# Kernel tuning notes

Hardware: AMD Instinct MI355X
Metric: run time of the kernel (lower is better)

## Reference

```python
import jax, jax.numpy as jnp
import numpy as np

D_MODEL = 512
NUM_HEADS = 8
D_HEAD = D_MODEL // NUM_HEADS
SCALE = 1.0 / np.sqrt(D_HEAD)


def setup_inputs() -> dict:
    key = jax.random.key(0)
    ks = jax.random.split(key, 16)
    B, T, D = 8, 1024, D_MODEL
    std = 1.0 / np.sqrt(D)
    inp = {
        'x': jax.random.normal(ks[0], (B, T, D), jnp.float32),
        'pos_enc': jax.random.normal(ks[1], (1, 2 * T - 1, D), jnp.float32),
        'Wq': jax.random.normal(ks[2], (D, D), jnp.float32) * std,
        'bq': jnp.zeros((D,), jnp.float32),
        'Wk': jax.random.normal(ks[3], (D, D), jnp.float32) * std,
        'bk': jnp.zeros((D,), jnp.float32),
        'Wv': jax.random.normal(ks[4], (D, D), jnp.float32) * std,
        'bv': jnp.zeros((D,), jnp.float32),
        'Wpos': jax.random.normal(ks[5], (D, D), jnp.float32) * std,
        'pos_bias_u': jax.random.normal(ks[6], (NUM_HEADS, D_HEAD), jnp.float32) * std,
        'pos_bias_v': jax.random.normal(ks[7], (NUM_HEADS, D_HEAD), jnp.float32) * std,
        'Wo': jax.random.normal(ks[8], (D, D), jnp.float32) * std,
        'bo': jnp.zeros((D,), jnp.float32),
    }
    return inp


def _relative_shift(x):
    # x: (batch, heads, time, 2*time-1) -> (batch, heads, time, time)
    b, h, t, _ = x.shape
    x = jnp.pad(x, ((0, 0), (0, 0), (0, 0), (1, 0)))  # (b,h,t,2t)
    x = x.reshape(b, h, 2 * t, t)
    x = x[:, :, 1:, :]
    x = x.reshape(b, h, t, 2 * t - 1)
    return x[:, :, :, :t]


def reference(x, pos_enc, Wq, bq, Wk, bk, Wv, bv, Wpos, pos_bias_u, pos_bias_v, Wo, bo):
    B, T, D = x.shape
    H, Dh = NUM_HEADS, D_HEAD
    q = (x @ Wq + bq).reshape(B, T, H, Dh).transpose(0, 2, 1, 3)  # (B,H,T,Dh)
    k = (x @ Wk + bk).reshape(B, T, H, Dh).transpose(0, 2, 1, 3)
    v = (x @ Wv + bv).reshape(B, T, H, Dh).transpose(0, 2, 1, 3)
    p = (pos_enc @ Wpos).reshape(1, -1, H, Dh).transpose(0, 2, 1, 3)  # (1,H,2T-1,Dh)

    q_u = q + pos_bias_u[None, :, None, :]
    q_v = q + pos_bias_v[None, :, None, :]

    content_score = jnp.einsum('bhtd,bhsd->bhts', q_u, k)         # (B,H,T,T)
    pos_score = jnp.einsum('bhtd,xhpd->bhtp', q_v, p)             # (B,H,T,2T-1)
    pos_score = _relative_shift(pos_score)                         # (B,H,T,T)

    scores = (content_score + pos_score) * SCALE
    attn = jax.nn.softmax(scores, axis=-1)
    out = jnp.einsum('bhts,bhsd->bhtd', attn, v)                   # (B,H,T,Dh)
    out = out.transpose(0, 2, 1, 3).reshape(B, T, D)
    return out @ Wo + bo
```

## Files before the change

kernel.cpp:

```cpp
#include <hip/hip_runtime.h>
#include <hip/hip_bf16.h>

#define T_SEQ 1024
#define D_MODEL 512
#define N_HEADS 8
#define D_HEAD 64
#define KSCALE 0.1803368801111244f

typedef unsigned short ushort_t;
typedef short s16x8 __attribute__((ext_vector_type(8)));
typedef float f32x4 __attribute__((ext_vector_type(4)));

__device__ inline f32x4 mfma16(s16x8 a, s16x8 b, f32x4 c) {
    return __builtin_amdgcn_mfma_f32_16x16x32_bf16(a, b, c, 0, 0, 0);
}

__device__ inline ushort_t f2bf(float f) {
    union { float f; unsigned u; } v; v.f = f;
    unsigned r = v.u + 0x7FFFu + ((v.u >> 16) & 1u);
    return (ushort_t)(r >> 16);
}
__device__ inline float bf2f(short s) {
    union { unsigned u; float f; } t; t.u = ((unsigned)(unsigned short)s) << 16; return t.f;
}
__device__ inline void cvt4(const float4 f, ushort_t* t) {
    t[0] = f2bf(f.x); t[1] = f2bf(f.y); t[2] = f2bf(f.z); t[3] = f2bf(f.w);
}
__device__ inline s16x8 pack8(const ushort_t* t) {
    s16x8 r;
    #pragma unroll
    for (int e = 0; e < 8; ++e) r[e] = (short)t[e];
    return r;
}

__device__ inline int lidx(int row, int chunk) {
    return row * 64 + ((chunk ^ (row & 7)) << 3);
}

__device__ inline void gl_lds16(const ushort_t* g, ushort_t* l) {
    __builtin_amdgcn_global_load_lds(
        (const __attribute__((address_space(1))) unsigned*)g,
        (__attribute__((address_space(3))) unsigned*)l, 16, 0, 0);
}

__global__ __launch_bounds__(256) void prep(
    const float* __restrict__ x, const float* __restrict__ pos,
    const float* __restrict__ W0, const float* __restrict__ W1,
    const float* __restrict__ W2, const float* __restrict__ W3,
    const float* __restrict__ W4,
    ushort_t* __restrict__ xb, ushort_t* __restrict__ posb,
    ushort_t* __restrict__ WT)
{
    __shared__ float T[64][68];
    const int bx = blockIdx.x;
    const int tid = threadIdx.x;
    if (bx < 2560) {
        const size_t N1 = (size_t)8192 * 512;
        size_t e = ((size_t)bx * 256 + tid) * 8;
        ushort_t tmp[8];
        if (e < N1) {
            const float4* s = (const float4*)(x + e);
            cvt4(s[0], tmp); cvt4(s[1], tmp + 4);
            *(s16x8*)(xb + e) = pack8(tmp);
        } else {
            size_t e2 = e - N1;
            int row = (int)(e2 >> 9);
            if (row < 2047) {
                const float4* s = (const float4*)(pos + e2);
                cvt4(s[0], tmp); cvt4(s[1], tmp + 4);
            } else {
                #pragma unroll
                for (int i = 0; i < 8; ++i) tmp[i] = 0;
            }
            *(s16x8*)(posb + e2) = pack8(tmp);
        }
    } else {
        const int bz = bx - 2560;
        const int z = bz >> 6;
        const int rem = bz & 63;
        const int n0 = (rem & 7) * 64, k0 = (rem >> 3) * 64;
        const float* W = (z == 0) ? W0 : (z == 1) ? W1
                       : (z == 2) ? W2 : (z == 3) ? W3 : W4;
        const int rr = tid >> 2, cc = (tid & 3) * 16;

        const float* src = W + (size_t)(k0 + rr) * 512 + n0 + cc;
        *(float4*)&T[rr][cc + 0]  = *(const float4*)(src);
        *(float4*)&T[rr][cc + 4]  = *(const float4*)(src + 4);
        *(float4*)&T[rr][cc + 8]  = *(const float4*)(src + 8);
        *(float4*)&T[rr][cc + 12] = *(const float4*)(src + 12);
        __syncthreads();

        ushort_t tmp[16];
        #pragma unroll
        for (int e = 0; e < 16; ++e) tmp[e] = f2bf(T[cc + e][rr]);
        ushort_t* dst = WT + ((size_t)z * 512 + n0 + rr) * 512 + k0 + cc;
        *(s16x8*)dst       = pack8(tmp);
        *(s16x8*)(dst + 8) = pack8(tmp + 8);
    }
}

__global__ __launch_bounds__(256) void gemm_qkvp(
    const ushort_t* __restrict__ xb, const ushort_t* __restrict__ posb,
    const ushort_t* __restrict__ WT,
    const float* __restrict__ bq, const float* __restrict__ bk,
    const float* __restrict__ bv, const float* __restrict__ pbu,
    ushort_t* __restrict__ Qu, ushort_t* __restrict__ Ko,
    ushort_t* __restrict__ VoT, ushort_t* __restrict__ Po)
{
    const int tid = threadIdx.x;
    const int flat = blockIdx.x;
    const int nf = (flat & 7) * 104 + (flat >> 3);
    const int bxi = nf % 13, byi = nf / 13;

    const bool is_p = (bxi == 12);
    int row0, col0;
    const ushort_t* A;
    const ushort_t* B;
    if (is_p) {
        row0 = (byi >> 2) * 128;
        col0 = (byi & 3) * 128;
        A = posb;
        B = WT + (size_t)3 * 512 * 512;
    } else {
        row0 = byi * 128;
        col0 = bxi * 128;
        A = xb;
        B = WT;
    }
    const int w = tid >> 6, lane = tid & 63;
    const int quad = lane >> 4, lanelo = lane & 15;
    const int wr = w >> 1, wc = w & 1;

    __shared__ ushort_t AsF[2][128 * 64];
    __shared__ ushort_t BsF[2][128 * 64];

    const int rs = tid >> 3, js = (tid & 7) * 8;
    const size_t lofs = (size_t)(tid & ~63) * 8;

    f32x4 acc[4][4] = {};

    #pragma unroll
    for (int i = 0; i < 4; ++i) {
        gl_lds16(A + (size_t)(row0 + i * 32 + rs) * 512 + js,
                 AsF[0] + (size_t)i * 2048 + lofs);
        gl_lds16(B + (size_t)(col0 + i * 32 + rs) * 512 + js,
                 BsF[0] + (size_t)i * 2048 + lofs);
    }

    for (int kk = 0; kk < 8; ++kk) {
        const int cur = kk & 1;
        __syncthreads();
        if (kk < 7) {
            const int k1 = (kk + 1) * 64;
            #pragma unroll
            for (int i = 0; i < 4; ++i) {
                gl_lds16(A + (size_t)(row0 + i * 32 + rs) * 512 + k1 + js,
                         AsF[cur ^ 1] + (size_t)i * 2048 + lofs);
                gl_lds16(B + (size_t)(col0 + i * 32 + rs) * 512 + k1 + js,
                         BsF[cur ^ 1] + (size_t)i * 2048 + lofs);
            }
        }
        const ushort_t* Ac = AsF[cur];
        const ushort_t* Bc = BsF[cur];
        #pragma unroll
        for (int ks = 0; ks < 2; ++ks) {
            s16x8 af[4], bf[4];
            #pragma unroll
            for (int i = 0; i < 4; ++i)
                af[i] = *(const s16x8*)(Ac + (size_t)(64 * wr + 16 * i + lanelo) * 64 + ks * 32 + quad * 8);
            #pragma unroll
            for (int j = 0; j < 4; ++j)
                bf[j] = *(const s16x8*)(Bc + (size_t)(64 * wc + 16 * j + lanelo) * 64 + ks * 32 + quad * 8);
            #pragma unroll
            for (int i = 0; i < 4; ++i)
                #pragma unroll
                for (int j = 0; j < 4; ++j)
                    acc[i][j] = mfma16(af[i], bf[j], acc[i][j]);
        }
    }

    if (is_p) {
        #pragma unroll
        for (int j = 0; j < 4; ++j) {
            int c = col0 + 64 * wc + 16 * j + lanelo;
            #pragma unroll
            for (int i = 0; i < 4; ++i)
                #pragma unroll
                for (int r = 0; r < 4; ++r) {
                    int row = row0 + 64 * wr + 16 * i + 4 * quad + r;
                    Po[(size_t)row * 512 + c] = f2bf(acc[i][j][r]);
                }
        }
        return;
    }

    const int set = col0 >> 9;
    const int cbase = (col0 & 511) + 64 * wc;
    if (set == 0) {
        #pragma unroll
        for (int j = 0; j < 4; ++j) {
            int c = cbase + 16 * j + lanelo;
            float vq = bq[c] + pbu[c];
            #pragma unroll
            for (int i = 0; i < 4; ++i)
                #pragma unroll
                for (int r = 0; r < 4; ++r) {
                    int row = row0 + 64 * wr + 16 * i + 4 * quad + r;
                    Qu[(size_t)row * 512 + c] = f2bf((acc[i][j][r] + vq) * KSCALE);
                }
        }
    } else if (set == 1) {
        #pragma unroll
        for (int j = 0; j < 4; ++j) {
            int c = cbase + 16 * j + lanelo;
            float vbk = bk[c];
            #pragma unroll
            for (int i = 0; i < 4; ++i)
                #pragma unroll
                for (int r = 0; r < 4; ++r) {
                    int row = row0 + 64 * wr + 16 * i + 4 * quad + r;
                    Ko[(size_t)row * 512 + c] = f2bf(acc[i][j][r] + vbk);
                }
        }
    } else {
        const int b_idx = row0 >> 10;
        #pragma unroll
        for (int j = 0; j < 4; ++j) {
            int c = cbase + 16 * j + lanelo;
            int hh = c >> 6, d = c & 63;
            float vbb = bv[c];
            #pragma unroll
            for (int i = 0; i < 4; ++i) {
                int t = (row0 & 1023) + 64 * wr + 16 * i + 4 * quad;
                ushort4 vp;
                vp.x = f2bf(acc[i][j][0] + vbb);
                vp.y = f2bf(acc[i][j][1] + vbb);
                vp.z = f2bf(acc[i][j][2] + vbb);
                vp.w = f2bf(acc[i][j][3] + vbb);
                *(ushort4*)(VoT + ((size_t)((b_idx * 8 + hh) * 64 + d)) * 1024 + t) = vp;
            }
        }
    }
}

__global__ __launch_bounds__(256, 2) void attn_mfma(
    const ushort_t* __restrict__ Qu,
    const ushort_t* __restrict__ Kb, const ushort_t* __restrict__ VT,
    const ushort_t* __restrict__ Pb,
    const float* __restrict__ pbu, const float* __restrict__ pbv,
    ushort_t* __restrict__ AOb)
{
    const int tid = threadIdx.x;
    const int flat = blockIdx.x;
    const int nf = (flat & 7) * 64 + (flat >> 3);
    const int t0 = (nf & 7) * 128;
    const int h  = (nf >> 3) & 7;
    const int b  = nf >> 6;

    const int w = tid >> 6, lane = tid & 63;
    const int quad = lane >> 4, lanelo = lane & 15;

    __shared__ ushort_t Kt[2 * 64 * 64];
    __shared__ ushort_t VtT[2 * 64 * 64];
    __shared__ ushort_t Pt[256 * 64];
    __shared__ ushort_t Ps[128 * 64];

    const size_t qr0 = (size_t)(b * T_SEQ + t0 + 32 * w + lanelo) * 512 + h * 64;
    s16x8 qu0[2], qu1[2], qv0[2], qv1[2];
    qu0[0] = *(const s16x8*)(Qu + qr0 + quad * 8);
    qu0[1] = *(const s16x8*)(Qu + qr0 + 32 + quad * 8);
    qu1[0] = *(const s16x8*)(Qu + qr0 + (size_t)16 * 512 + quad * 8);
    qu1[1] = *(const s16x8*)(Qu + qr0 + (size_t)16 * 512 + 32 + quad * 8);
    #pragma unroll
    for (int e = 0; e < 8; ++e) {
        int k0i = h * 64 + quad * 8 + e;
        float d0 = (pbv[k0i] - pbu[k0i]) * KSCALE;
        float d1 = (pbv[k0i + 32] - pbu[k0i + 32]) * KSCALE;
        qv0[0][e] = (short)f2bf(bf2f(qu0[0][e]) + d0);
        qv0[1][e] = (short)f2bf(bf2f(qu0[1][e]) + d1);
        qv1[0][e] = (short)f2bf(bf2f(qu1[0][e]) + d0);
        qv1[1][e] = (short)f2bf(bf2f(qu1[1][e]) + d1);
    }

    f32x4 acc_o[2][4] = {};
    float l_part[2][4] = {{0.f,0.f,0.f,0.f},{0.f,0.f,0.f,0.f}};

    const ushort_t* VTbh = VT + ((size_t)((b * 8 + h) * 64)) * 1024;
    const ushort_t* Kbh  = Kb + (size_t)b * T_SEQ * 512 + (size_t)h * 64;
    const int pr_base = 960 - t0;

    {
        #pragma unroll
        for (int i = 0; i < 2; ++i) {
            const int L = i * 256 + tid;
            const int r = L >> 3;
            const int ch = (L & 7) ^ (r & 7);
            gl_lds16(Kbh + (size_t)r * 512 + ch * 8,
                     Kt + (size_t)(i * 256 + (tid & ~63)) * 8);
            gl_lds16(VTbh + (size_t)r * 1024 + ch * 8,
                     VtT + (size_t)(i * 256 + (tid & ~63)) * 8);
        }
        const int g0p = pr_base - 64;
        #pragma unroll
        for (int i = 0; i < 6; ++i) {
            const int L = i * 256 + tid;
            const int gr = g0p + (L >> 3);
            const int ch = (L & 7) ^ (gr & 7);
            const int sgb = (g0p + ((i * 256 + (tid & ~63)) >> 3)) & 255;
            gl_lds16(Pb + (size_t)gr * 512 + h * 64 + ch * 8,
                     Pt + (size_t)sgb * 64);
        }
    }
    __syncthreads();

    for (int it = 0; it < 16; ++it) {
        const int s0 = it * 64;
        const int cur = it & 1;

        if (it < 15) {
            ushort_t* Kn = Kt + (cur ^ 1) * 4096;
            ushort_t* Vn = VtT + (cur ^ 1) * 4096;
            const int sn = s0 + 64;
            #pragma unroll
            for (int i = 0; i < 2; ++i) {
                const int L = i * 256 + tid;
                const int r = L >> 3;
                const int ch = (L & 7) ^ (r & 7);
                gl_lds16(Kbh + (size_t)(sn + r) * 512 + ch * 8,
                         Kn + (size_t)(i * 256 + (tid & ~63)) * 8);
                gl_lds16(VTbh + (size_t)r * 1024 + sn + ch * 8,
                         Vn + (size_t)(i * 256 + (tid & ~63)) * 8);
            }
            const int g0 = pr_base + s0 + 128;
            #pragma unroll
            for (int i = 0; i < 2; ++i) {
                const int L = i * 256 + tid;
                const int gr = g0 + (L >> 3);
                const int ch = (L & 7) ^ (gr & 7);
                const int sgb = (g0 + ((i * 256 + (tid & ~63)) >> 3)) & 255;
                gl_lds16(Pb + (size_t)gr * 512 + h * 64 + ch * 8,
                         Pt + (size_t)sgb * 64);
            }
        }

        const ushort_t* Kc = Kt + cur * 4096;
        const ushort_t* Vc = VtT + cur * 4096;
        const int pb = (pr_base + s0) & 255;

        f32x4 acc_c[2][4] = {};
        f32x4 acc_g[2][5] = {};
        __builtin_amdgcn_s_setprio(1);
        #pragma unroll
        for (int ks = 0; ks < 2; ++ks) {
            #pragma unroll
            for (int tn = 0; tn < 4; ++tn) {
                s16x8 kf = *(const s16x8*)(Kc + lidx(tn * 16 + lanelo, 4 * ks + quad));
                acc_c[0][tn] = mfma16(qu0[ks], kf, acc_c[0][tn]);
                acc_c[1][tn] = mfma16(qu1[ks], kf, acc_c[1][tn]);
            }
            #pragma unroll
            for (int m = 0; m < 6; ++m) {
                int prow = (pb + 256 + (2 - 2 * w + m) * 16 + lanelo) & 255;
                s16x8 pf = *(const s16x8*)(Pt + lidx(prow, 4 * ks + quad));
                if (m >= 1) acc_g[0][m - 1] = mfma16(qv0[ks], pf, acc_g[0][m - 1]);
                if (m <= 4) acc_g[1][m]     = mfma16(qv1[ks], pf, acc_g[1][m]);
            }
        }
        __builtin_amdgcn_s_setprio(0);

        #pragma unroll
        for (int rt = 0; rt < 2; ++rt) {
            #pragma unroll
            for (int r = 0; r < 4; ++r) {
                const int u = lanelo + 15 - 4 * quad - r;
                const int srcl = (quad << 4) | (u & 15);
                const bool hi = (u >= 16);
                #pragma unroll
                for (int tn = 0; tn < 4; ++tn) {
                    float v0 = __shfl(acc_g[rt][tn][r], srcl);
                    float v1 = __shfl(acc_g[rt][tn + 1][r], srcl);
                    float e = __builtin_amdgcn_exp2f(acc_c[rt][tn][r] + (hi ? v1 : v0));
                    l_part[rt][r] += e;
                    const int pr = 32 * w + 16 * rt + 4 * quad + r;
                    const int ch = 2 * tn + (lanelo >> 3);
                    Ps[pr * 64 + ((ch ^ (pr & 7)) << 3) + (lanelo & 7)] = f2bf(e);
                }
            }
        }
        asm volatile("s_waitcnt lgkmcnt(0)" ::: "memory");

        __builtin_amdgcn_s_setprio(1);
        #pragma unroll
        for (int ks = 0; ks < 2; ++ks) {
            s16x8 af0 = *(const s16x8*)(Ps + lidx(32 * w + lanelo, 4 * ks + quad));
            s16x8 af1 = *(const s16x8*)(Ps + lidx(32 * w + 16 + lanelo, 4 * ks + quad));
            #pragma unroll
            for (int dt = 0; dt < 4; ++dt) {
                s16x8 vb = *(const s16x8*)(Vc + lidx(dt * 16 + lanelo, 4 * ks + quad));
                acc_o[0][dt] = mfma16(af0, vb, acc_o[0][dt]);
                acc_o[1][dt] = mfma16(af1, vb, acc_o[1][dt]);
            }
        }
        __builtin_amdgcn_s_setprio(0);

        __syncthreads();
    }

    float inv[2][4];
    #pragma unroll
    for (int rt = 0; rt < 2; ++rt)
        #pragma unroll
        for (int r = 0; r < 4; ++r) {
            float l = l_part[rt][r];
            l += __shfl_xor(l, 1);
            l += __shfl_xor(l, 2);
            l += __shfl_xor(l, 4);
            l += __shfl_xor(l, 8);
            inv[rt][r] = 1.0f / l;
        }

    #pragma unroll
    for (int rt = 0; rt < 2; ++rt)
        #pragma unroll
        for (int dt = 0; dt < 4; ++dt)
            #pragma unroll
            for (int r = 0; r < 4; ++r) {
                const int pr = 32 * w + 16 * rt + 4 * quad + r;
                const int ch = 2 * dt + (lanelo >> 3);
                Ps[pr * 64 + ((ch ^ (pr & 7)) << 3) + (lanelo & 7)] =
                    f2bf(acc_o[rt][dt][r] * inv[rt][r]);
            }
    __syncthreads();
    {
        const int row = tid >> 1, cb = (tid & 1) * 4;
        ushort_t* dst = AOb + (size_t)(b * T_SEQ + t0 + row) * 512 + h * 64 + cb * 8;
        #pragma unroll
        for (int c = 0; c < 4; ++c)
            *(s16x8*)(dst + c * 8) = *(const s16x8*)(Ps + lidx(row, cb + c));
    }
}

__global__ __launch_bounds__(256) void gemm_out(
    const ushort_t* __restrict__ A, const ushort_t* __restrict__ WTo,
    const float* __restrict__ bias, float* __restrict__ C)
{
    const int tid = threadIdx.x;
    const int flat = blockIdx.x;
    const int nfi = (flat & 7) * 32 + (flat >> 3);
    const int col0 = (nfi & 3) * 128;
    const int row0 = (nfi >> 2) * 128;
    const int w = tid >> 6, lane = tid & 63;
    const int quad = lane >> 4, lanelo = lane & 15;
    const int wr = w >> 1, wc = w & 1;

    __shared__ ushort_t AsF[2][128 * 64];
    __shared__ ushort_t BsF[2][128 * 64];

    const int rs = tid >> 3, js = (tid & 7) * 8;
    const size_t lofs = (size_t)(tid & ~63) * 8;

    f32x4 acc[4][4] = {};

    #pragma unroll
    for (int i = 0; i < 4; ++i) {
        gl_lds16(A + (size_t)(row0 + i * 32 + rs) * 512 + js,
                 AsF[0] + (size_t)i * 2048 + lofs);
        gl_lds16(WTo + (size_t)(col0 + i * 32 + rs) * 512 + js,
                 BsF[0] + (size_t)i * 2048 + lofs);
    }

    for (int kk = 0; kk < 8; ++kk) {
        const int cur = kk & 1;
        __syncthreads();
        if (kk < 7) {
            const int k1 = (kk + 1) * 64;
            #pragma unroll
            for (int i = 0; i < 4; ++i) {
                gl_lds16(A + (size_t)(row0 + i * 32 + rs) * 512 + k1 + js,
                         AsF[cur ^ 1] + (size_t)i * 2048 + lofs);
                gl_lds16(WTo + (size_t)(col0 + i * 32 + rs) * 512 + k1 + js,
                         BsF[cur ^ 1] + (size_t)i * 2048 + lofs);
            }
        }
        const ushort_t* Ac = AsF[cur];
        const ushort_t* Bc = BsF[cur];
        #pragma unroll
        for (int ks = 0; ks < 2; ++ks) {
            s16x8 af[4], bf[4];
            #pragma unroll
            for (int i = 0; i < 4; ++i)
                af[i] = *(const s16x8*)(Ac + (size_t)(64 * wr + 16 * i + lanelo) * 64 + ks * 32 + quad * 8);
            #pragma unroll
            for (int j = 0; j < 4; ++j)
                bf[j] = *(const s16x8*)(Bc + (size_t)(64 * wc + 16 * j + lanelo) * 64 + ks * 32 + quad * 8);
            #pragma unroll
            for (int i = 0; i < 4; ++i)
                #pragma unroll
                for (int j = 0; j < 4; ++j)
                    acc[i][j] = mfma16(af[i], bf[j], acc[i][j]);
        }
    }

    #pragma unroll
    for (int j = 0; j < 4; ++j) {
        int c = col0 + 64 * wc + 16 * j + lanelo;
        float vb = bias[c];
        #pragma unroll
        for (int i = 0; i < 4; ++i)
            #pragma unroll
            for (int r = 0; r < 4; ++r) {
                int row = row0 + 64 * wr + 16 * i + 4 * quad + r;
                C[(size_t)row * 512 + c] = acc[i][j][r] + vb;
            }
    }
}

extern "C" void kernel_launch(void* const* d_in, const int* in_sizes, int n_in,
                              void* d_out, int out_size, void* d_ws, size_t ws_size,
                              hipStream_t stream) {
    const float* x       = (const float*)d_in[0];
    const float* pos_enc = (const float*)d_in[1];
    const float* Wq      = (const float*)d_in[2];
    const float* bq      = (const float*)d_in[3];
    const float* Wk      = (const float*)d_in[4];
    const float* bk      = (const float*)d_in[5];
    const float* Wv      = (const float*)d_in[6];
    const float* bv      = (const float*)d_in[7];
    const float* Wpos    = (const float*)d_in[8];
    const float* pbu     = (const float*)d_in[9];
    const float* pbv     = (const float*)d_in[10];
    const float* Wo      = (const float*)d_in[11];
    const float* bo      = (const float*)d_in[12];
    float* out = (float*)d_out;

    const size_t M  = 8 * T_SEQ;
    const size_t SZ = M * D_MODEL;

    char* ws = (char*)d_ws;
    ushort_t* xb   = (ushort_t*)ws;              ws += SZ * 2;
    ushort_t* posb = (ushort_t*)ws;              ws += (size_t)2048 * 512 * 2;
    ushort_t* Qu_b = (ushort_t*)ws;              ws += SZ * 2;
    ushort_t* K_b  = (ushort_t*)ws;              ws += SZ * 2;
    ushort_t* VT_b = (ushort_t*)ws;              ws += SZ * 2;
    ushort_t* P_b  = (ushort_t*)ws;              ws += (size_t)2048 * 512 * 2;
    ushort_t* WT   = (ushort_t*)ws;              ws += (size_t)5 * 512 * 512 * 2;
    ushort_t* AOb  = (ushort_t*)ws;              ws += SZ * 2;

    dim3 blk(256);

    hipLaunchKernelGGL(prep, dim3(2880), blk, 0, stream,
                       x, pos_enc, Wq, Wk, Wv, Wpos, Wo, xb, posb, WT);

    hipLaunchKernelGGL(gemm_qkvp, dim3(832), blk, 0, stream,
                       xb, posb, WT, bq, bk, bv, pbu,
                       Qu_b, K_b, VT_b, P_b);

    hipLaunchKernelGGL(attn_mfma, dim3(512), blk, 0, stream,
                       Qu_b, K_b, VT_b, P_b, pbu, pbv, AOb);

    hipLaunchKernelGGL(gemm_out, dim3(256), blk, 0, stream,
                       AOb, WT + (size_t)4 * 512 * 512, bo, out);
}
```

Measured before the change: 186.3 us.

## Load K, V and positional fragments directly from global instead of LDS staging

Removes the double-buffered LDS staging of the K, V and positional-projection tiles, along with the per-iteration block barrier. Each wave now reads its MFMA operand fragments straight from global memory through per-lane base pointers, and V fragments are loaded before the softmax phase to hide latency. The goal is to cut LDS traffic and barrier stalls and to free shared memory for higher occupancy. The cost is that each wave fetches redundant, row-strided data through the caches, and the loads are no longer prefetched an iteration ahead. A smaller change hoists the relative-shift shuffles so each value is shuffled once instead of twice.

```diff
diff --git a/kernel.cpp b/kernel.cpp
--- a/kernel.cpp
+++ b/kernel.cpp
@@ -260,9 +260,6 @@
     const int w = tid >> 6, lane = tid & 63;
     const int quad = lane >> 4, lanelo = lane & 15;
 
-    __shared__ ushort_t Kt[2 * 64 * 64];
-    __shared__ ushort_t VtT[2 * 64 * 64];
-    __shared__ ushort_t Pt[256 * 64];
     __shared__ ushort_t Ps[128 * 64];
 
     const size_t qr0 = (size_t)(b * T_SEQ + t0 + 32 * w + lanelo) * 512 + h * 64;
@@ -285,67 +282,16 @@
     f32x4 acc_o[2][4] = {};
     float l_part[2][4] = {{0.f,0.f,0.f,0.f},{0.f,0.f,0.f,0.f}};
 
-    const ushort_t* VTbh = VT + ((size_t)((b * 8 + h) * 64)) * 1024;
-    const ushort_t* Kbh  = Kb + (size_t)b * T_SEQ * 512 + (size_t)h * 64;
+    const ushort_t* Kfl = Kb + (size_t)b * T_SEQ * 512 + (size_t)h * 64
+                        + (size_t)lanelo * 512 + quad * 8;
+    const ushort_t* Vfl = VT + ((size_t)((b * 8 + h) * 64)) * 1024
+                        + (size_t)lanelo * 1024 + quad * 8;
     const int pr_base = 960 - t0;
-
-    {
-        #pragma unroll
-        for (int i = 0; i < 2; ++i) {
-            const int L = i * 256 + tid;
-            const int r = L >> 3;
-            const int ch = (L & 7) ^ (r & 7);
-            gl_lds16(Kbh + (size_t)r * 512 + ch * 8,
-                     Kt + (size_t)(i * 256 + (tid & ~63)) * 8);
-            gl_lds16(VTbh + (size_t)r * 1024 + ch * 8,
-                     VtT + (size_t)(i * 256 + (tid & ~63)) * 8);
-        }
-        const int g0p = pr_base - 64;
-        #pragma unroll
-        for (int i = 0; i < 6; ++i) {
-            const int L = i * 256 + tid;
-            const int gr = g0p + (L >> 3);
-            const int ch = (L & 7) ^ (gr & 7);
-            const int sgb = (g0p + ((i * 256 + (tid & ~63)) >> 3)) & 255;
-            gl_lds16(Pb + (size_t)gr * 512 + h * 64 + ch * 8,
-                     Pt + (size_t)sgb * 64);
-        }
-    }
-    __syncthreads();
+    const ushort_t* Pfl = Pb + (size_t)(pr_base + (2 - 2 * w) * 16 + lanelo) * 512
+                        + h * 64 + quad * 8;
 
     for (int it = 0; it < 16; ++it) {
         const int s0 = it * 64;
-        const int cur = it & 1;
-
-        if (it < 15) {
-            ushort_t* Kn = Kt + (cur ^ 1) * 4096;
-            ushort_t* Vn = VtT + (cur ^ 1) * 4096;
-            const int sn = s0 + 64;
-            #pragma unroll
-            for (int i = 0; i < 2; ++i) {
-                const int L = i * 256 + tid;
-                const int r = L >> 3;
-                const int ch = (L & 7) ^ (r & 7);
-                gl_lds16(Kbh + (size_t)(sn + r) * 512 + ch * 8,
-                         Kn + (size_t)(i * 256 + (tid & ~63)) * 8);
-                gl_lds16(VTbh + (size_t)r * 1024 + sn + ch * 8,
-                         Vn + (size_t)(i * 256 + (tid & ~63)) * 8);
-            }
-            const int g0 = pr_base + s0 + 128;
-            #pragma unroll
-            for (int i = 0; i < 2; ++i) {
-                const int L = i * 256 + tid;
-                const int gr = g0 + (L >> 3);
-                const int ch = (L & 7) ^ (gr & 7);
-                const int sgb = (g0 + ((i * 256 + (tid & ~63)) >> 3)) & 255;
-                gl_lds16(Pb + (size_t)gr * 512 + h * 64 + ch * 8,
-                         Pt + (size_t)sgb * 64);
-            }
-        }
-
-        const ushort_t* Kc = Kt + cur * 4096;
-        const ushort_t* Vc = VtT + cur * 4096;
-        const int pb = (pr_base + s0) & 255;
 
         f32x4 acc_c[2][4] = {};
         f32x4 acc_g[2][5] = {};
@@ -354,19 +300,25 @@
         for (int ks = 0; ks < 2; ++ks) {
             #pragma unroll
             for (int tn = 0; tn < 4; ++tn) {
-                s16x8 kf = *(const s16x8*)(Kc + lidx(tn * 16 + lanelo, 4 * ks + quad));
+                s16x8 kf = *(const s16x8*)(Kfl + (size_t)(s0 + 16 * tn) * 512 + ks * 32);
                 acc_c[0][tn] = mfma16(qu0[ks], kf, acc_c[0][tn]);
                 acc_c[1][tn] = mfma16(qu1[ks], kf, acc_c[1][tn]);
             }
             #pragma unroll
             for (int m = 0; m < 6; ++m) {
-                int prow = (pb + 256 + (2 - 2 * w + m) * 16 + lanelo) & 255;
-                s16x8 pf = *(const s16x8*)(Pt + lidx(prow, 4 * ks + quad));
+                s16x8 pf = *(const s16x8*)(Pfl + (size_t)(s0 + 16 * m) * 512 + ks * 32);
                 if (m >= 1) acc_g[0][m - 1] = mfma16(qv0[ks], pf, acc_g[0][m - 1]);
                 if (m <= 4) acc_g[1][m]     = mfma16(qv1[ks], pf, acc_g[1][m]);
             }
         }
         __builtin_amdgcn_s_setprio(0);
+
+        s16x8 vb[2][4];
+        #pragma unroll
+        for (int ks = 0; ks < 2; ++ks)
+            #pragma unroll
+            for (int dt = 0; dt < 4; ++dt)
+                vb[ks][dt] = *(const s16x8*)(Vfl + (size_t)(16 * dt) * 1024 + s0 + ks * 32);
 
         #pragma unroll
         for (int rt = 0; rt < 2; ++rt) {
@@ -375,11 +327,12 @@
                 const int u = lanelo + 15 - 4 * quad - r;
                 const int srcl = (quad << 4) | (u & 15);
                 const bool hi = (u >= 16);
+                float sv[5];
+                #pragma unroll
+                for (int m = 0; m < 5; ++m) sv[m] = __shfl(acc_g[rt][m][r], srcl);
                 #pragma unroll
                 for (int tn = 0; tn < 4; ++tn) {
-                    float v0 = __shfl(acc_g[rt][tn][r], srcl);
-                    float v1 = __shfl(acc_g[rt][tn + 1][r], srcl);
-                    float e = __builtin_amdgcn_exp2f(acc_c[rt][tn][r] + (hi ? v1 : v0));
+                    float e = __builtin_amdgcn_exp2f(acc_c[rt][tn][r] + (hi ? sv[tn + 1] : sv[tn]));
                     l_part[rt][r] += e;
                     const int pr = 32 * w + 16 * rt + 4 * quad + r;
                     const int ch = 2 * tn + (lanelo >> 3);
@@ -387,7 +340,6 @@
                 }
             }
         }
-        asm volatile("s_waitcnt lgkmcnt(0)" ::: "memory");
 
         __builtin_amdgcn_s_setprio(1);
         #pragma unroll
@@ -396,14 +348,11 @@
             s16x8 af1 = *(const s16x8*)(Ps + lidx(32 * w + 16 + lanelo, 4 * ks + quad));
             #pragma unroll
             for (int dt = 0; dt < 4; ++dt) {
-                s16x8 vb = *(const s16x8*)(Vc + lidx(dt * 16 + lanelo, 4 * ks + quad));
-                acc_o[0][dt] = mfma16(af0, vb, acc_o[0][dt]);
-                acc_o[1][dt] = mfma16(af1, vb, acc_o[1][dt]);
+                acc_o[0][dt] = mfma16(af0, vb[ks][dt], acc_o[0][dt]);
+                acc_o[1][dt] = mfma16(af1, vb[ks][dt], acc_o[1][dt]);
             }
         }
         __builtin_amdgcn_s_setprio(0);
-
-        __syncthreads();
     }
 
     float inv[2][4];
```

Measured after the change: 286.5 us. 1.54x slower.
